# Optimization experiments

Measured on AMD Instinct MI355X. Metric: run time of the kernel, lower is better.

## Reference

```python
import jax, jax.numpy as jnp
import numpy as np

SCORE_THRESHOLD = 0.3
MAX_DET = 300


def _nms_keep(boxes, valid, iou_thresh):
    # Greedy NMS. boxes [N,4] already sorted desc by score and class-offset;
    # valid [N] bool marks entries passing the score threshold.
    x1, y1, x2, y2 = boxes[:, 0], boxes[:, 1], boxes[:, 2], boxes[:, 3]
    areas = jnp.maximum(x2 - x1, 0.0) * jnp.maximum(y2 - y1, 0.0)
    N = boxes.shape[0]
    idx = jnp.arange(N)

    def body(i, keep):
        bi = boxes[i]
        xx1 = jnp.maximum(bi[0], x1)
        yy1 = jnp.maximum(bi[1], y1)
        xx2 = jnp.minimum(bi[2], x2)
        yy2 = jnp.minimum(bi[3], y2)
        inter = jnp.maximum(xx2 - xx1, 0.0) * jnp.maximum(yy2 - yy1, 0.0)
        iou = inter / (areas[i] + areas - inter + 1e-9)
        suppress = (iou > iou_thresh) & (idx > i) & keep[i]
        return keep & (~suppress)

    return jax.lax.fori_loop(0, N, body, valid)


def setup_inputs() -> dict:
    key = jax.random.key(0)
    k1, k2, k3, k4 = jax.random.split(key, 4)
    B, N = 16, 4096
    img = 512.0
    # plausible boxes: centers in [0, 512], sizes in [10, 100]
    cxy = jax.random.uniform(k1, (B, N, 2)) * img
    wh = jax.random.uniform(k2, (B, N, 2)) * 90.0 + 10.0
    boxes = jnp.concatenate([cxy - wh / 2.0, cxy + wh / 2.0], axis=-1)
    scores = jax.random.uniform(k3, (B, N))
    labels = jax.random.randint(k4, (B, N), 0, 2, dtype=jnp.int32)
    nms_thresh = jnp.float32(-0.6)
    class_weights = jnp.ones((2,), jnp.float32)
    return {"boxes": boxes, "scores": scores, "labels": labels,
            "nms_thresh": nms_thresh, "class_weights": class_weights,
            "img_size": 512}


def reference(boxes, scores, labels, nms_thresh, class_weights, img_size):
    B, N, _ = boxes.shape
    fimg = jnp.asarray(img_size, boxes.dtype)
    boxes = jnp.clip(boxes, 0.0, fimg)  # clamp all 4 coords to [0, img_size]
    valid = scores > SCORE_THRESHOLD
    weighted = scores * class_weights[labels]
    # sort each batch by weighted score, invalid entries pushed to the end
    sort_key = jnp.where(valid, weighted, -jnp.inf)
    order = jnp.argsort(-sort_key, axis=1)
    sb = jnp.take_along_axis(boxes, order[..., None], axis=1)   # [B,N,4]
    ss = jnp.take_along_axis(scores, order, axis=1)             # original scores
    sl = jnp.take_along_axis(labels, order, axis=1)
    sv = jnp.take_along_axis(valid, order, axis=1)
    iou_thresh = jax.nn.sigmoid(nms_thresh)
    # batched_nms trick: offset boxes per class so cross-class IoU is 0
    ob = sb + sl.astype(sb.dtype)[..., None] * (fimg + 1.0)
    keep = jax.vmap(_nms_keep, in_axes=(0, 0, None))(ob, sv, iou_thresh)  # [B,N]
    # compact kept detections (score order preserved) into padded [B, MAX_DET]
    rank = jnp.cumsum(keep, axis=1) - 1
    pos = jnp.where(keep & (rank < MAX_DET), rank, MAX_DET)  # overflow slot MAX_DET
    brow = jnp.arange(B)[:, None]
    out_boxes = jnp.zeros((B, MAX_DET + 1, 4), sb.dtype).at[brow, pos].set(sb)[:, :MAX_DET]
    out_scores = jnp.zeros((B, MAX_DET + 1), ss.dtype).at[brow, pos].set(ss)[:, :MAX_DET]
    out_labels = jnp.zeros((B, MAX_DET + 1), sl.dtype).at[brow, pos].set(sl)[:, :MAX_DET]
    out_valid = jnp.zeros((B, MAX_DET + 1), bool).at[brow, pos].set(keep)[:, :MAX_DET]
    return out_boxes, out_scores, out_labels, out_valid
```

## Files before the change

### kernel.cpp

```cpp
#include <hip/hip_runtime.h>
#include <math.h>

#define NBOX   4096
#define NTHR   1024
#define MAXDET 300
#define CAP    3968
#define NWORDS (NBOX / 32)

typedef unsigned long long ull;

__device__ __forceinline__ float clipf(float v, float hi) {
  return fminf(fmaxf(v, 0.0f), hi);
}

__device__ __forceinline__ float getimg(const int* img_i) {
  int iv = *img_i;
  return (iv > 0 && iv < (1 << 24)) ? (float)iv : __int_as_float(iv);
}

#define CSWAP_REG(va, vb, eo, K) { int e_ = wbase + (eo) + lane;                     \
    if ((((e_) & (K)) == 0) ? ((va) < (vb)) : ((va) > (vb))) { ull t_=(va); (va)=(vb); (vb)=t_; } }
#define CSWAP_SHFL(vr, eo, K) { int e_ = wbase + (eo) + lane;                        \
    ull c_ = __shfl_xor((vr), j);                                                    \
    bool km_ = ((((e_) & (K)) == 0) == ((lane & j) == 0));                           \
    (vr) = km_ ? ((vr) > c_ ? (vr) : c_) : ((vr) < c_ ? (vr) : c_); }
#define LOCALPHASES(jmax, K) { for (int j = (jmax); j >= 1; j >>= 1) {               \
    if (j == 128)      { CSWAP_REG(v0, v2, 0, K);  CSWAP_REG(v1, v3, 64, K);  }      \
    else if (j == 64)  { CSWAP_REG(v0, v1, 0, K);  CSWAP_REG(v2, v3, 128, K); }      \
    else { CSWAP_SHFL(v0, 0, K); CSWAP_SHFL(v1, 64, K); CSWAP_SHFL(v2, 128, K); CSWAP_SHFL(v3, 192, K); } } }

__device__ __forceinline__ void emit_one(ull key, int l, int b, int N,
    const float* boxes, const int* labels, float fimg, float offs,
    int* ws_sorted, float4* obox, float* area)
{
  unsigned orig = 0xFFFFFFFFu - (unsigned)(key & 0xFFFFFFFFull);
  ws_sorted[(size_t)b * N + l] = (int)orig;
  const float4* bx4 = (const float4*)(boxes + (size_t)b * N * 4);
  float4 bb = bx4[orig];
  float off = (float)labels[(size_t)b * N + orig] * offs;
  bb.x = clipf(bb.x, fimg) + off;
  bb.y = clipf(bb.y, fimg) + off;
  bb.z = clipf(bb.z, fimg) + off;
  bb.w = clipf(bb.w, fimg) + off;
  obox[(size_t)b * NBOX + l] = bb;
  area[(size_t)b * NBOX + l] = fmaxf(bb.z - bb.x, 0.0f) * fmaxf(bb.w - bb.y, 0.0f);
}

__global__ __launch_bounds__(256)
void sort_seg(const float* __restrict__ scores,
              const int*   __restrict__ labels,
              const float* __restrict__ cls_w,
              ull* __restrict__ ws_keys,
              int* __restrict__ ws_Vseg,
              int N)
{
  __shared__ ull ks[1024];
  __shared__ int cnt;
  const int b = blockIdx.y, s = blockIdx.x;
  const int tid = threadIdx.x, lane = tid & 63, wave = tid >> 6;
  const int wbase = wave * 256;
  const int base  = s * 1024;
  const float* sc = scores + (size_t)b * N;
  const int*   lb = labels + (size_t)b * N;
  if (tid == 0) cnt = 0;

  ull v0, v1, v2, v3;
  int vc = 0;
  #define BUILD(vm, mo) { int l_ = wbase + (mo) + lane; int gi = base + l_;          \
      float sv = sc[gi]; ull key = (ull)(0xFFFFFFFFu - (unsigned)gi);                \
      if (sv > 0.3f) { float w_ = sv * cls_w[lb[gi]]; unsigned ub = __float_as_uint(w_); \
        ub = (ub & 0x80000000u) ? ~ub : (ub | 0x80000000u);                          \
        key |= ((ull)ub << 32); ++vc; }                                              \
      vm = key; }
  BUILD(v0, 0) BUILD(v1, 64) BUILD(v2, 128) BUILD(v3, 192)
  #undef BUILD
  atomicAdd(&cnt, vc);

  for (int k2 = 2; k2 <= 256; k2 <<= 1) { LOCALPHASES(k2 >> 1, k2); }

  #define STV { ks[wbase + lane] = v0; ks[wbase + 64 + lane] = v1;                   \
                ks[wbase + 128 + lane] = v2; ks[wbase + 192 + lane] = v3; }
  #define LDV { v0 = ks[wbase + lane]; v1 = ks[wbase + 64 + lane];                   \
                v2 = ks[wbase + 128 + lane]; v3 = ks[wbase + 192 + lane]; }
  #define CROSS(J, K) { for (int i = tid; i < 1024; i += 256) { int l2 = i ^ (J);    \
      if (l2 > i) { ull a = ks[i], c = ks[l2];                                       \
        if ((((i) & (K)) == 0) ? (a < c) : (a > c)) { ks[i] = c; ks[l2] = a; } } } }

  STV; __syncthreads();
  CROSS(256, 512); __syncthreads();
  LDV; LOCALPHASES(128, 512);
  STV; __syncthreads();
  CROSS(512, 1024); __syncthreads();
  CROSS(256, 1024); __syncthreads();
  LDV; LOCALPHASES(128, 1024);

  ull* kb = ws_keys + (size_t)b * NBOX + base;
  kb[wbase + lane]       = v0;
  kb[wbase + 64 + lane]  = v1;
  kb[wbase + 128 + lane] = v2;
  kb[wbase + 192 + lane] = v3;
  __syncthreads();
  if (tid == 0) ws_Vseg[b * 4 + s] = cnt;
  #undef STV
  #undef LDV
  #undef CROSS
}

__global__ __launch_bounds__(512)
void merge_top(const ull* __restrict__ ws_keys,
               const int* __restrict__ ws_Vseg,
               const float* __restrict__ boxes,
               const int*   __restrict__ labels,
               const int*   __restrict__ img_i,
               int*    __restrict__ ws_sorted,
               int*    __restrict__ ws_V,
               int*    __restrict__ ws_done,
               float4* __restrict__ obox,
               float*  __restrict__ area,
               int N)
{
  __shared__ ull ksh[2][1024];
  const int b = blockIdx.x;
  const int tid = threadIdx.x, lane = tid & 63, wave = tid >> 6;
  const int g = wave >> 2, wv = wave & 3;
  const int wbase = wv * 256;
  const ull* kb = ws_keys + (size_t)b * NBOX;

  ull v0, v1, v2, v3;
  #define PMAX(vm, mo) { int l_ = wbase + (mo) + lane;                               \
      ull a = kb[g * 2048 + l_]; ull c = kb[g * 2048 + 1024 + (1023 - l_)];          \
      vm = (a > c) ? a : c; }
  PMAX(v0, 0) PMAX(v1, 64) PMAX(v2, 128) PMAX(v3, 192)
  #undef PMAX

  #define STVG(arr) { (arr)[wbase + lane] = v0; (arr)[wbase + 64 + lane] = v1;       \
                      (arr)[wbase + 128 + lane] = v2; (arr)[wbase + 192 + lane] = v3; }
  #define LDVG(arr) { v0 = (arr)[wbase + lane]; v1 = (arr)[wbase + 64 + lane];       \
                      v2 = (arr)[wbase + 128 + lane]; v3 = (arr)[wbase + 192 + lane]; }
  #define MCROSS(arr, J) { for (int i = (tid & 255); i < 1024; i += 256) {           \
      int l2 = i ^ (J); if (l2 > i) { ull a = (arr)[i], c = (arr)[l2];               \
        if (a < c) { (arr)[i] = c; (arr)[l2] = a; } } } }

  STVG(ksh[g]); __syncthreads();
  MCROSS(ksh[g], 512); __syncthreads();
  MCROSS(ksh[g], 256); __syncthreads();
  LDVG(ksh[g]); LOCALPHASES(128, 2048);
  STVG(ksh[g]); __syncthreads();

  if (g == 0) {
    #define PMAX2(vm, mo) { int l_ = wbase + (mo) + lane;                            \
        ull a = ksh[0][l_]; ull c = ksh[1][1023 - l_]; vm = (a > c) ? a : c; }
    PMAX2(v0, 0) PMAX2(v1, 64) PMAX2(v2, 128) PMAX2(v3, 192)
    #undef PMAX2
  }
  __syncthreads();
  if (g == 0) STVG(ksh[0]);
  __syncthreads();
  if (tid < 256) MCROSS(ksh[0], 512);
  __syncthreads();
  if (tid < 256) MCROSS(ksh[0], 256);
  __syncthreads();

  if (g == 0) {
    LDVG(ksh[0]); LOCALPHASES(128, 2048);
    float fimg = getimg(img_i);
    float offs = fimg + 1.0f;
    emit_one(v0, wbase + lane,       b, N, boxes, labels, fimg, offs, ws_sorted, obox, area);
    emit_one(v1, wbase + 64 + lane,  b, N, boxes, labels, fimg, offs, ws_sorted, obox, area);
    emit_one(v2, wbase + 128 + lane, b, N, boxes, labels, fimg, offs, ws_sorted, obox, area);
    emit_one(v3, wbase + 192 + lane, b, N, boxes, labels, fimg, offs, ws_sorted, obox, area);
  }
  if (tid == 0) {
    ws_V[b] = ws_Vseg[b * 4] + ws_Vseg[b * 4 + 1] + ws_Vseg[b * 4 + 2] + ws_Vseg[b * 4 + 3];
    ws_done[b] = 0;
  }
  #undef STVG
  #undef LDVG
  #undef MCROSS
}

__global__ __launch_bounds__(256)
void suptr0(const float4* __restrict__ obox,
            const float*  __restrict__ area,
            const float*  __restrict__ nms_th,
            const int*    __restrict__ ws_V,
            ull* __restrict__ trans)
{
  __shared__ float4 rbox[64];
  __shared__ float  rarea[64];
  __shared__ ull    part[4][64];
  const int b = blockIdx.y;
  int rem = blockIdx.x, d = 0;
  while (rem >= d + 1) { rem -= d + 1; ++d; }
  const int jt = d, w = rem;
  const int V = ws_V[b];
  if (jt * 64 >= V) return;
  const int JW = (V + 63) >> 6;
  if (w >= JW) return;

  const int tid = threadIdx.x, wave = tid >> 6, lane = tid & 63;
  double xt = (double)(*nms_th);
  float  th = (float)(1.0 / (1.0 + exp(-xt)));
  const float4* ob = obox + (size_t)b * NBOX;
  const float*  ar = area + (size_t)b * NBOX;

  if (tid < 64) { rbox[tid] = ob[w * 64 + tid]; rarea[tid] = ar[w * 64 + tid]; }
  __syncthreads();

  const int j = jt * 64 + lane;
  const float4 bj = ob[j];
  const float  aj = ar[j];
  ull p = 0;
  #pragma unroll 4
  for (int rr = 0; rr < 16; ++rr) {
    const int r = wave * 16 + rr;
    const int i = w * 64 + r;
    const float4 bi = rbox[r];
    const float  ai = rarea[r];
    float xx1 = fmaxf(bi.x, bj.x);
    float yy1 = fmaxf(bi.y, bj.y);
    float xx2 = fminf(bi.z, bj.z);
    float yy2 = fminf(bi.w, bj.w);
    float inter = fmaxf(xx2 - xx1, 0.0f) * fmaxf(yy2 - yy1, 0.0f);
    float denom = ai + aj;
    denom = denom - inter;
    denom = denom + 1e-9f;
    float iou = inter / denom;
    bool cond = (iou > th) && (j > i);
    p |= cond ? (1ull << r) : 0ull;
  }
  part[wave][lane] = p;
  __syncthreads();
  if (tid < 64)
    trans[(size_t)b * 16 * NBOX + (size_t)w * NBOX + jt * 64 + tid] =
        (part[0][tid] | part[1][tid]) | (part[2][tid] | part[3][tid]);
}

__global__ __launch_bounds__(NTHR)
void resolve0(const float* __restrict__ boxes,
              const float* __restrict__ scores,
              const int*   __restrict__ labels,
              const int*   __restrict__ img_i,
              const int*   __restrict__ ws_V,
              const ull*   __restrict__ trans,
              int* __restrict__ ws_done,
              int* __restrict__ ws_total,
              ull* __restrict__ ws_keptw,
              int* __restrict__ ws_K,
              const int* __restrict__ ws_sorted,
              float* __restrict__ out,
              int B, int N)
{
  __shared__ ull aw[16];
  __shared__ ull kw[16];
  __shared__ int kept_sh[MAXDET];
  __shared__ int flag, fin, Ktot;

  const int b = blockIdx.x;
  const int tid = threadIdx.x, wave = tid >> 6, lane = tid & 63;
  const int V = ws_V[b], JW = (V + 63) >> 6;
  const int j = tid;
  const ull* tb = trans + (size_t)b * 16 * NBOX;

  ull supT[16];
  #pragma unroll
  for (int w = 0; w < 16; ++w)
    supT[w] = (w <= wave) ? tb[(size_t)w * NBOX + j] : 0ull;

  const bool a0 = (j < V);
  { ull bw0 = __ballot(a0); if (lane == 0) aw[wave] = bw0; }
  __syncthreads();

  for (;;) {
    ull s = 0;
    #pragma unroll
    for (int w = 0; w < 16; ++w) s |= aw[w] & supT[w];
    const bool keep = a0 && (s == 0ull);
    const ull bw = __ballot(keep);
    const bool diff = (lane == 0) && (bw != aw[wave]);
    __syncthreads();
    if (tid == 0) flag = 0;
    __syncthreads();
    if (diff) { aw[wave] = bw; flag = 1; }
    __syncthreads();
    if (!flag) break;
  }

  if (wave == 0) {
    ull w64 = (lane < 16) ? aw[lane] : 0ull;
    int pc = __popcll(w64), incl = pc;
    #pragma unroll
    for (int s2 = 1; s2 < 64; s2 <<= 1) { int v = __shfl_up(incl, s2); if (lane >= s2) incl += v; }
    const int totalALL = __shfl(incl, 63);
    const bool fi = (totalALL >= MAXDET) || (16 >= JW);
    if (fi) {
      int cumprev = incl - pc;
      int room = MAXDET - cumprev; if (room < 0) room = 0;
      int nk = (room < pc) ? room : pc;
      if (nk == 0) w64 = 0;
      else while (pc > nk) { int msb = 63 - __builtin_clzll(w64); w64 &= ~(1ull << msb); --pc; }
    }
    if (lane < 16) { kw[lane] = w64; ws_keptw[(size_t)b * 64 + lane] = w64; }
    if (lane == 0) { fin = fi ? 1 : 0; Ktot = (totalALL < MAXDET) ? totalALL : MAXDET; }
  }
  __syncthreads();

  if (!fin) { if (tid == 0) ws_total[b] = Ktot; return; }

  if (wave == 0) {
    ull km = (lane < 16) ? kw[lane] : 0ull;
    int pc = __popcll(km), incl = pc;
    #pragma unroll
    for (int s2 = 1; s2 < 64; s2 <<= 1) { int v = __shfl_up(incl, s2); if (lane >= s2) incl += v; }
    int base = incl - pc;
    while (km) { int l = __builtin_ctzll(km); km &= km - 1; kept_sh[base++] = lane * 64 + l; }
  }
  __syncthreads();

  const int K = Ktot;
  float fimg = getimg(img_i);
  const float* bx = boxes  + (size_t)b * N * 4;
  const float* sc = scores + (size_t)b * N;
  const int*   lb = labels + (size_t)b * N;
  const int*   so = ws_sorted + (size_t)b * N;
  float4* obx = (float4*)out;
  float*  osc = out + (size_t)B * MAXDET * 4;
  float*  olb = osc + (size_t)B * MAXDET;
  float*  ovl = olb + (size_t)B * MAXDET;
  for (int rI = tid; rI < MAXDET; rI += NTHR) {
    size_t slot = (size_t)b * MAXDET + rI;
    if (rI < K) {
      int i    = kept_sh[rI];
      int orig = so[i];
      float4 bb = ((const float4*)bx)[orig];
      bb.x = clipf(bb.x, fimg);
      bb.y = clipf(bb.y, fimg);
      bb.z = clipf(bb.z, fimg);
      bb.w = clipf(bb.w, fimg);
      obx[slot] = bb;
      osc[slot] = sc[orig];
      olb[slot] = (float)lb[orig];
      ovl[slot] = 1.0f;
    } else {
      obx[slot] = make_float4(0.f, 0.f, 0.f, 0.f);
      osc[slot] = 0.0f;
      olb[slot] = 0.0f;
      ovl[slot] = 0.0f;
    }
  }
  if (tid == 0) { ws_K[b] = K; ws_done[b] = 1; }
}

__global__ __launch_bounds__(NTHR)
void cleanup_kernel(const ull* __restrict__ ws_keys,
                    const float* __restrict__ boxes,
                    const float* __restrict__ scores,
                    const int*   __restrict__ labels,
                    const int*   __restrict__ img_i,
                    const float* __restrict__ nms_th,
                    const int* __restrict__ ws_V,
                    int* __restrict__ ws_done,
                    const int* __restrict__ ws_total,
                    const ull* __restrict__ ws_keptw,
                    const float4* __restrict__ obox,
                    int* __restrict__ ws_K,
                    float* __restrict__ out,
                    int B, int N)
{
  __shared__ ull    K[4096];
  __shared__ float4 rb[1024];
  __shared__ float  ra[1024];
  __shared__ float4 kbox[MAXDET];
  __shared__ float  karea[MAXDET];
  __shared__ ull    aw[16];
  __shared__ ull    kw[64];
  __shared__ int    kept_sh[MAXDET];
  __shared__ int    flag, fin, Ktot;

  const int b = blockIdx.x;
  if (ws_done[b]) return;
  const int tid = threadIdx.x, wave = tid >> 6, lane = tid & 63;
  const int V = ws_V[b], JW = (V + 63) >> 6;
  float fimg = getimg(img_i);
  float offs = fimg + 1.0f;
  double xt = (double)(*nms_th);
  float th = (float)(1.0 / (1.0 + exp(-xt)));

  const ull* kb = ws_keys + (size_t)b * NBOX;
  for (int i = tid; i < 4096; i += NTHR) K[i] = kb[i];
  __syncthreads();
  { int i = tid;
    { ull a = K[i], c = K[2047 - i];        if (a < c) { K[i] = c; K[2047 - i] = a; } }
    { ull a = K[2048 + i], c = K[4095 - i]; if (a < c) { K[2048 + i] = c; K[4095 - i] = a; } } }
  __syncthreads();
  for (int j2 = 512; j2 >= 1; j2 >>= 1) {
    for (int idx = tid; idx < 4096; idx += NTHR) {
      int l = idx ^ j2;
      if (l > idx) { ull a = K[idx], c = K[l]; if (a < c) { K[idx] = c; K[l] = a; } } }
    __syncthreads(); }
  for (int m = 0; m < 2; ++m) {
    int i2 = tid + m * NTHR;
    ull a = K[i2], c = K[4095 - i2];
    if (a < c) { K[i2] = c; K[4095 - i2] = a; } }
  __syncthreads();
  for (int j2 = 1024; j2 >= 1; j2 >>= 1) {
    for (int idx = tid; idx < 4096; idx += NTHR) {
      int l = idx ^ j2;
      if (l > idx) { ull a = K[idx], c = K[l]; if (a < c) { K[idx] = c; K[l] = a; } } }
    __syncthreads(); }

  int total = ws_total[b];
  const ull* kwg = ws_keptw + (size_t)b * 64;
  if (tid < 64) kw[tid] = (tid < 16) ? kwg[tid] : 0ull;
  __syncthreads();
  if (wave == 0) {
    ull km = (lane < 16) ? kw[lane] : 0ull;
    int pc = __popcll(km), incl = pc;
    #pragma unroll
    for (int s2 = 1; s2 < 64; s2 <<= 1) { int v = __shfl_up(incl, s2); if (lane >= s2) incl += v; }
    int base = incl - pc;
    while (km) { int l = __builtin_ctzll(km); km &= km - 1; kept_sh[base++] = lane * 64 + l; }
  }
  __syncthreads();
  for (int k = tid; k < total; k += NTHR) {
    float4 bb = obox[(size_t)b * NBOX + kept_sh[k]];
    kbox[k]  = bb;
    karea[k] = fmaxf(bb.z - bb.x, 0.0f) * fmaxf(bb.w - bb.y, 0.0f);
  }
  __syncthreads();

  for (int c = 1; c < 4; ++c) {
    const int t0 = 16 * c, t1 = t0 + 16;
    {
      int gi = t0 * 64 + tid;
      unsigned orig = 0xFFFFFFFFu - (unsigned)(K[gi] & 0xFFFFFFFFull);
      float4 bb = ((const float4*)(boxes + (size_t)b * N * 4))[orig];
      float off = (float)labels[(size_t)b * N + orig] * offs;
      bb.x = clipf(bb.x, fimg) + off;
      bb.y = clipf(bb.y, fimg) + off;
      bb.z = clipf(bb.z, fimg) + off;
      bb.w = clipf(bb.w, fimg) + off;
      rb[tid] = bb;
      ra[tid] = fmaxf(bb.z - bb.x, 0.0f) * fmaxf(bb.w - bb.y, 0.0f);
    }
    __syncthreads();

    const int j = t0 * 64 + tid;
    const float4 bj = rb[tid];
    const float  aj = ra[tid];

    ull supT[16];
    for (int w = 0; w < 16; ++w) {
      ull word = 0;
      if (w <= wave) {
        for (int rr = 0; rr < 64; ++rr) {
          const int lr = w * 64 + rr;
          const float4 bi = rb[lr];
          const float  ai = ra[lr];
          float xx1 = fmaxf(bi.x, bj.x);
          float yy1 = fmaxf(bi.y, bj.y);
          float xx2 = fminf(bi.z, bj.z);
          float yy2 = fminf(bi.w, bj.w);
          float inter = fmaxf(xx2 - xx1, 0.0f) * fmaxf(yy2 - yy1, 0.0f);
          float denom = ai + aj;
          denom = denom - inter;
          denom = denom + 1e-9f;
          float iou = inter / denom;
          bool cond = (iou > th) && (tid > lr);
          word |= cond ? (1ull << rr) : 0ull;
        }
      }
      supT[w] = word;
    }
    bool cat = false;
    for (int k = 0; k < total && !cat; ++k) {
      const float4 bi = kbox[k];
      const float  ai = karea[k];
      float xx1 = fmaxf(bi.x, bj.x);
      float yy1 = fmaxf(bi.y, bj.y);
      float xx2 = fminf(bi.z, bj.z);
      float yy2 = fminf(bi.w, bj.w);
      float inter = fmaxf(xx2 - xx1, 0.0f) * fmaxf(yy2 - yy1, 0.0f);
      float denom = ai + aj;
      denom = denom - inter;
      denom = denom + 1e-9f;
      float iou = inter / denom;
      if (iou > th) cat = true;
    }
    const bool a0 = (j < V) && !cat;
    { ull bw0 = __ballot(a0); if (lane == 0) aw[wave] = bw0; }
    __syncthreads();

    for (;;) {
      ull s = 0;
      #pragma unroll
      for (int w = 0; w < 16; ++w) s |= aw[w] & supT[w];
      const bool keep = a0 && (s == 0ull);
      const ull bw = __ballot(keep);
      const bool diff = (lane == 0) && (bw != aw[wave]);
      __syncthreads();
      if (tid == 0) flag = 0;
      __syncthreads();
      if (diff) { aw[wave] = bw; flag = 1; }
      __syncthreads();
      if (!flag) break;
    }

    if (wave == 0) {
      ull w64 = (lane < 16) ? aw[lane] : 0ull;
      int pc = __popcll(w64), incl = pc;
      #pragma unroll
      for (int s2 = 1; s2 < 64; s2 <<= 1) { int v = __shfl_up(incl, s2); if (lane >= s2) incl += v; }
      const int totalALL = total + __shfl(incl, 63);
      const bool fi = (totalALL >= MAXDET) || (t1 >= JW);
      if (fi) {
        int cumprev = total + incl - pc;
        int room = MAXDET - cumprev; if (room < 0) room = 0;
        int nk = (room < pc) ? room : pc;
        if (nk == 0) { w64 = 0; pc = 0; }
        else while (pc > nk) { int msb = 63 - __builtin_clzll(w64); w64 &= ~(1ull << msb); --pc; }
      }
      if (lane < 16) kw[t0 + lane] = w64;
      if (lane == 0) { fin = fi ? 1 : 0; Ktot = (totalALL < MAXDET) ? totalALL : MAXDET; }
    }
    __syncthreads();

    if (wave == 0) {
      ull km = (lane < 16) ? kw[t0 + lane] : 0ull;
      int pc = __popcll(km), incl = pc;
      #pragma unroll
      for (int s2 = 1; s2 < 64; s2 <<= 1) { int v = __shfl_up(incl, s2); if (lane >= s2) incl += v; }
      int base = total + incl - pc;
      while (km) { int l = __builtin_ctzll(km); km &= km - 1; kept_sh[base++] = (t0 + lane) * 64 + l; }
    }
    __syncthreads();
    const int newtotal = Ktot;
    for (int k = total + tid; k < newtotal; k += NTHR) {
      int lr = kept_sh[k] - t0 * 64;
      kbox[k]  = rb[lr];
      karea[k] = ra[lr];
    }
    total = newtotal;
    __syncthreads();
    if (fin) break;
  }

  const int Kf = total;
  const float* bx = boxes  + (size_t)b * N * 4;
  const float* sc = scores + (size_t)b * N;
  const int*   lb = labels + (size_t)b * N;
  float4* obx = (float4*)out;
  float*  osc = out + (size_t)B * MAXDET * 4;
  float*  olb = osc + (size_t)B * MAXDET;
  float*  ovl = olb + (size_t)B * MAXDET;
  for (int rI = tid; rI < MAXDET; rI += NTHR) {
    size_t slot = (size_t)b * MAXDET + rI;
    if (rI < Kf) {
      int i = kept_sh[rI];
      unsigned orig = 0xFFFFFFFFu - (unsigned)(K[i] & 0xFFFFFFFFull);
      float4 bb = ((const float4*)bx)[orig];
      bb.x = clipf(bb.x, fimg);
      bb.y = clipf(bb.y, fimg);
      bb.z = clipf(bb.z, fimg);
      bb.w = clipf(bb.w, fimg);
      obx[slot] = bb;
      osc[slot] = sc[orig];
      olb[slot] = (float)lb[orig];
      ovl[slot] = 1.0f;
    } else {
      obx[slot] = make_float4(0.f, 0.f, 0.f, 0.f);
      osc[slot] = 0.0f;
      olb[slot] = 0.0f;
      ovl[slot] = 0.0f;
    }
  }
  if (tid == 0) { ws_K[b] = Kf; ws_done[b] = 1; }
}

__global__ __launch_bounds__(NTHR)
void merge_full(const ull* __restrict__ ws_keys,
                const float* __restrict__ boxes,
                const int*   __restrict__ labels,
                const int*   __restrict__ img_i,
                int*    __restrict__ ws_sorted,
                float4* __restrict__ obox,
                float*  __restrict__ area,
                int N)
{
  __shared__ ull K[4096];
  const int b = blockIdx.x;
  const int tid = threadIdx.x;
  const ull* kb = ws_keys + (size_t)b * NBOX;
  for (int i = tid; i < 4096; i += NTHR) K[i] = kb[i];
  __syncthreads();
  { int i = tid;
    { ull a = K[i], c = K[2047 - i];        if (a < c) { K[i] = c; K[2047 - i] = a; } }
    { ull a = K[2048 + i], c = K[4095 - i]; if (a < c) { K[2048 + i] = c; K[4095 - i] = a; } } }
  __syncthreads();
  for (int j = 512; j >= 1; j >>= 1) {
    for (int idx = tid; idx < 4096; idx += NTHR) {
      int l = idx ^ j;
      if (l > idx) { ull a = K[idx], c = K[l]; if (a < c) { K[idx] = c; K[l] = a; } } }
    __syncthreads(); }
  for (int m = 0; m < 2; ++m) {
    int i2 = tid + m * 1024;
    ull a = K[i2], c = K[4095 - i2];
    if (a < c) { K[i2] = c; K[4095 - i2] = a; } }
  __syncthreads();
  for (int j = 1024; j >= 1; j >>= 1) {
    for (int idx = tid; idx < 4096; idx += NTHR) {
      int l = idx ^ j;
      if (l > idx) { ull a = K[idx], c = K[l]; if (a < c) { K[idx] = c; K[l] = a; } } }
    __syncthreads(); }

  float fimg = getimg(img_i);
  float offs = fimg + 1.0f;
  for (int idx = 1024 + tid; idx < 4096; idx += NTHR)
    emit_one(K[idx], idx, b, N, boxes, labels, fimg, offs, ws_sorted, obox, area);
}

struct SMB {
  float4       obox[CAP];
  unsigned int keepw[NWORDS];
  int          kept_pos[MAXDET];
  int          scal[4];
};

__global__ __launch_bounds__(NTHR)
void nms_kernel(const float* __restrict__ boxes,
                const float* __restrict__ scores,
                const int*   __restrict__ labels,
                const float* __restrict__ nms_th,
                const float* __restrict__ cls_w,
                const int*   __restrict__ img_i,
                float* __restrict__ out,
                int B, int N,
                const int* __restrict__ ws_sorted,
                const int* __restrict__ ws_V,
                float4* __restrict__ ws_ovf)
{
  __shared__ SMB sm;
  const int b    = blockIdx.x;
  const int tid  = threadIdx.x;

  const float* bx = boxes  + (size_t)b * N * 4;
  const float* sc = scores + (size_t)b * N;
  const int*   lb = labels + (size_t)b * N;
  const int*   so = ws_sorted + (size_t)b * N;

  float fimg = getimg(img_i);
  float off_scale = fimg + 1.0f;
  double xt = (double)(*nms_th);
  float  th = (float)(1.0 / (1.0 + exp(-xt)));

  const int V = ws_V[b];
  if (tid < 4) sm.scal[tid] = 0;

  for (int m = 0; m < 4; ++m) {
    int i = tid + m * NTHR;
    int orig = so[i];
    float4 bb = ((const float4*)bx)[orig];
    float off = (float)lb[orig] * off_scale;
    bb.x = clipf(bb.x, fimg) + off;
    bb.y = clipf(bb.y, fimg) + off;
    bb.z = clipf(bb.z, fimg) + off;
    bb.w = clipf(bb.w, fimg) + off;
    if (i < CAP) sm.obox[i] = bb;
    else         ws_ovf[(size_t)b * (NBOX - CAP) + (i - CAP)] = bb;
  }
  for (int w = tid; w < NWORDS; w += NTHR) {
    int lo = w * 32;
    unsigned val;
    if      (V >= lo + 32) val = 0xFFFFFFFFu;
    else if (V <= lo)      val = 0u;
    else                   val = (1u << (V - lo)) - 1u;
    sm.keepw[w] = val;
  }
  __syncthreads();

  const int nt = (V + 63) >> 6;
  int TR = 0;
  for (int t = 0; t < nt; ++t) {
    if (tid < 64) {
      int i0 = t * 64;
      int me = i0 + tid;
      float4 bb = (me < CAP) ? sm.obox[me]
                             : ws_ovf[(size_t)b * (NBOX - CAP) + (me - CAP)];
      float arJ = fmaxf(bb.z - bb.x, 0.0f) * fmaxf(bb.w - bb.y, 0.0f);
      ull supby = 0;
      for (int l = 0; l < 64; ++l) {
        int i = i0 + l;
        float4 bi = (i < CAP) ? sm.obox[i]
                              : ws_ovf[(size_t)b * (NBOX - CAP) + (i - CAP)];
        float ai = fmaxf(bi.z - bi.x, 0.0f) * fmaxf(bi.w - bi.y, 0.0f);
        float xx1 = fmaxf(bi.x, bb.x);
        float yy1 = fmaxf(bi.y, bb.y);
        float xx2 = fminf(bi.z, bb.z);
        float yy2 = fminf(bi.w, bb.w);
        float inter = fmaxf(xx2 - xx1, 0.0f) * fmaxf(yy2 - yy1, 0.0f);
        float denom = ai + arJ;
        denom = denom - inter;
        denom = denom + 1e-9f;
        float iou = inter / denom;
        if (iou > th) supby |= (1ull << l);
      }
      ull alive = ((ull)sm.keepw[2 * t + 1] << 32) | sm.keepw[2 * t];
      ull rem = alive;
      while (rem) {
        int l = __builtin_ctzll(rem);
        rem &= rem - 1;
        ull sup = __ballot((supby >> l) & 1ull);
        sup &= ((~1ull) << l);
        sup &= alive;
        alive &= ~sup;
        rem   &= ~sup;
      }
      if (tid == 0) {
        sm.keepw[2 * t]     = (unsigned)alive;
        sm.keepw[2 * t + 1] = (unsigned)(alive >> 32);
        atomicAdd(&sm.scal[1], __builtin_popcountll(alive));
      }
    }
    __syncthreads();
    TR = t + 1;
    if (sm.scal[1] >= MAXDET) break;

    int jstart = (t + 1) * 64;
    if (jstart < V) {
      ull alive = ((ull)sm.keepw[2 * t + 1] << 32) | sm.keepw[2 * t];
      if (alive) {
        for (int j = jstart + tid; j < V; j += NTHR) {
          unsigned wj = sm.keepw[j >> 5];
          if (!((wj >> (j & 31)) & 1u)) continue;
          float4 bj = (j < CAP) ? sm.obox[j]
                                : ws_ovf[(size_t)b * (NBOX - CAP) + (j - CAP)];
          float aj = fmaxf(bj.z - bj.x, 0.0f) * fmaxf(bj.w - bj.y, 0.0f);
          ull rem = alive;
          bool suppressed = false;
          while (rem) {
            int l = __builtin_ctzll(rem);
            rem &= rem - 1;
            int i = t * 64 + l;
            float4 bi = (i < CAP) ? sm.obox[i]
                                  : ws_ovf[(size_t)b * (NBOX - CAP) + (i - CAP)];
            float ai = fmaxf(bi.z - bi.x, 0.0f) * fmaxf(bi.w - bi.y, 0.0f);
            float xx1 = fmaxf(bi.x, bj.x);
            float yy1 = fmaxf(bi.y, bj.y);
            float xx2 = fminf(bi.z, bj.z);
            float yy2 = fminf(bi.w, bj.w);
            float inter = fmaxf(xx2 - xx1, 0.0f) * fmaxf(yy2 - yy1, 0.0f);
            float denom = ai + aj;
            denom = denom - inter;
            denom = denom + 1e-9f;
            float iou = inter / denom;
            if (iou > th) { suppressed = true; break; }
          }
          if (suppressed) atomicAnd(&sm.keepw[j >> 5], ~(1u << (j & 31)));
        }
      }
    }
    __syncthreads();
  }

  if (tid < NWORDS && tid >= TR * 2) sm.keepw[tid] = 0;
  __syncthreads();
  if (tid == 0) {
    int r = 0;
    for (int w = 0; w < NWORDS && r < MAXDET; ++w) {
      unsigned bits = sm.keepw[w];
      while (bits && r < MAXDET) {
        int l = __builtin_ctz(bits);
        bits &= bits - 1;
        sm.kept_pos[r++] = w * 32 + l;
      }
    }
    sm.scal[3] = r;
  }
  __syncthreads();
  const int K = sm.scal[3];

  float4* obx = (float4*)out;
  float*  osc = out + (size_t)B * MAXDET * 4;
  float*  olb = osc + (size_t)B * MAXDET;
  float*  ovl = olb + (size_t)B * MAXDET;
  for (int r = tid; r < MAXDET; r += NTHR) {
    size_t slot = (size_t)b * MAXDET + r;
    if (r < K) {
      int i    = sm.kept_pos[r];
      int orig = so[i];
      float4 bb = ((const float4*)bx)[orig];
      bb.x = clipf(bb.x, fimg);
      bb.y = clipf(bb.y, fimg);
      bb.z = clipf(bb.z, fimg);
      bb.w = clipf(bb.w, fimg);
      obx[slot] = bb;
      osc[slot] = sc[orig];
      olb[slot] = (float)lb[orig];
      ovl[slot] = 1.0f;
    } else {
      obx[slot] = make_float4(0.f, 0.f, 0.f, 0.f);
      osc[slot] = 0.0f;
      olb[slot] = 0.0f;
      ovl[slot] = 0.0f;
    }
  }
}

extern "C" void kernel_launch(void* const* d_in, const int* in_sizes, int n_in,
                              void* d_out, int out_size, void* d_ws, size_t ws_size,
                              hipStream_t stream) {
  const float* boxes      = (const float*)d_in[0];
  const float* scores     = (const float*)d_in[1];
  const int*   labels     = (const int*)d_in[2];
  const float* nms_thresh = (const float*)d_in[3];
  const float* cls_w      = (const float*)d_in[4];
  const int*   img_sz     = (const int*)d_in[5];

  int B = out_size / (MAXDET * 7);
  int N = in_sizes[1] / B;

  size_t off_sorted = 0;
  size_t off_V      = (off_sorted + (size_t)B * N * 4 + 255) & ~(size_t)255;
  size_t off_Vseg   = off_V + (size_t)B * 4;
  size_t off_done   = off_Vseg + (size_t)B * 16;
  size_t off_total  = off_done + (size_t)B * 4;
  size_t off_Kf     = off_total + (size_t)B * 4;
  size_t off_kw     = (off_Kf + (size_t)B * 4 + 255) & ~(size_t)255;
  size_t off_obox   = (off_kw + (size_t)B * 64 * 8 + 255) & ~(size_t)255;
  size_t off_area   = off_obox + (size_t)B * NBOX * 16;
  size_t off_keys   = (off_area + (size_t)B * NBOX * 4 + 255) & ~(size_t)255;
  size_t off_tr     = (off_keys + (size_t)B * NBOX * 8 + 255) & ~(size_t)255;
  size_t sz_tr      = (size_t)B * 16 * NBOX * 8;
  size_t need_fast  = off_tr + sz_tr;

  int*    ws_sorted = (int*)((char*)d_ws + off_sorted);
  int*    ws_V      = (int*)((char*)d_ws + off_V);
  int*    ws_Vseg   = (int*)((char*)d_ws + off_Vseg);
  int*    ws_done   = (int*)((char*)d_ws + off_done);
  int*    ws_total  = (int*)((char*)d_ws + off_total);
  int*    ws_K      = (int*)((char*)d_ws + off_Kf);
  ull*    ws_keptw  = (ull*)((char*)d_ws + off_kw);
  float4* obox      = (float4*)((char*)d_ws + off_obox);
  float*  area      = (float*)((char*)d_ws + off_area);
  ull*    ws_keys   = (ull*)((char*)d_ws + off_keys);
  ull*    trans     = (ull*)((char*)d_ws + off_tr);

  if (ws_size >= need_fast && N == NBOX) {
    sort_seg<<<dim3(4, B), dim3(256), 0, stream>>>(scores, labels, cls_w,
                                                   ws_keys, ws_Vseg, N);
    merge_top<<<dim3(B), dim3(512), 0, stream>>>(ws_keys, ws_Vseg, boxes, labels,
                                                 img_sz, ws_sorted, ws_V, ws_done,
                                                 obox, area, N);
    suptr0<<<dim3(136, B), dim3(256), 0, stream>>>(
        obox, area, nms_thresh, ws_V, trans);
    resolve0<<<dim3(B), dim3(NTHR), 0, stream>>>(
        boxes, scores, labels, img_sz, ws_V, trans,
        ws_done, ws_total, ws_keptw, ws_K, ws_sorted, (float*)d_out, B, N);
    cleanup_kernel<<<dim3(B), dim3(NTHR), 0, stream>>>(
        ws_keys, boxes, scores, labels, img_sz, nms_thresh, ws_V,
        ws_done, ws_total, ws_keptw, obox, ws_K, (float*)d_out, B, N);
  } else {
    sort_seg<<<dim3(4, B), dim3(256), 0, stream>>>(scores, labels, cls_w,
                                                   ws_keys, ws_Vseg, N);
    merge_top<<<dim3(B), dim3(512), 0, stream>>>(ws_keys, ws_Vseg, boxes, labels,
                                                 img_sz, ws_sorted, ws_V, ws_done,
                                                 obox, area, N);
    merge_full<<<dim3(B), dim3(NTHR), 0, stream>>>(
        ws_keys, boxes, labels, img_sz, ws_sorted, obox, area, N);
    float4* ws_ovf = (float4*)((char*)d_ws + off_keys);
    nms_kernel<<<dim3(B), dim3(NTHR), 0, stream>>>(boxes, scores, labels,
                                                   nms_thresh, cls_w, img_sz,
                                                   (float*)d_out, B, N,
                                                   ws_sorted, ws_V, ws_ovf);
  }
}
```

Baseline: 58.56 us.

## Fuse segment sort and top merge into one kernel; double-buffer resolve flags

Merges the per-segment bitonic sort and the top-k merge into a single 1024-thread block per batch, so the merge reads sorted keys from shared memory instead of global memory and one kernel launch is removed. Valid counts now stay in shared memory rather than going through a workspace array. Separately, the resolve loop uses double-buffered alive masks and __syncthreads_or, which cuts three barriers per iteration down to one. The trade-off is only 16 blocks for the sort stage (previously 64), which lowers parallelism, and a larger shared memory footprint.

```diff
diff --git a/kernel.cpp b/kernel.cpp
--- a/kernel.cpp
+++ b/kernel.cpp
@@ -46,27 +46,40 @@
   area[(size_t)b * NBOX + l] = fmaxf(bb.z - bb.x, 0.0f) * fmaxf(bb.w - bb.y, 0.0f);
 }
 
-__global__ __launch_bounds__(256)
-void sort_seg(const float* __restrict__ scores,
-              const int*   __restrict__ labels,
-              const float* __restrict__ cls_w,
-              ull* __restrict__ ws_keys,
-              int* __restrict__ ws_Vseg,
-              int N)
+__global__ __launch_bounds__(NTHR)
+void sort_merge(const float* __restrict__ scores,
+                const int*   __restrict__ labels,
+                const float* __restrict__ cls_w,
+                const float* __restrict__ boxes,
+                const int*   __restrict__ img_i,
+                ull* __restrict__ ws_keys,
+                int* __restrict__ ws_sorted,
+                int* __restrict__ ws_V,
+                int* __restrict__ ws_done,
+                float4* __restrict__ obox,
+                float*  __restrict__ area,
+                int N)
 {
-  __shared__ ull ks[1024];
-  __shared__ int cnt;
-  const int b = blockIdx.y, s = blockIdx.x;
-  const int tid = threadIdx.x, lane = tid & 63, wave = tid >> 6;
-  const int wbase = wave * 256;
-  const int base  = s * 1024;
+  __shared__ ull ks[4096];
+  __shared__ ull ksh[2][1024];
+  __shared__ int cnt[4];
+
+  const int b = blockIdx.x;
+  const int tid = threadIdx.x;
+  const int lane = tid & 63;
+  const int wave = tid >> 6;
+  const int wv = wave & 3;
+  const int wbase = wv * 256;
+  const int s = tid >> 8;
+  const int gtid = tid & 255;
   const float* sc = scores + (size_t)b * N;
   const int*   lb = labels + (size_t)b * N;
-  if (tid == 0) cnt = 0;
+
+  if (tid < 4) cnt[tid] = 0;
 
   ull v0, v1, v2, v3;
   int vc = 0;
-  #define BUILD(vm, mo) { int l_ = wbase + (mo) + lane; int gi = base + l_;          \
+  #define BUILD(vm, mo) { int l_ = wbase + (mo) + lane; int gi = s * 1024 + l_;      \
       float sv = sc[gi]; ull key = (ull)(0xFFFFFFFFu - (unsigned)gi);                \
       if (sv > 0.3f) { float w_ = sv * cls_w[lb[gi]]; unsigned ub = __float_as_uint(w_); \
         ub = (ub & 0x80000000u) ? ~ub : (ub | 0x80000000u);                          \
@@ -74,64 +87,40 @@
       vm = key; }
   BUILD(v0, 0) BUILD(v1, 64) BUILD(v2, 128) BUILD(v3, 192)
   #undef BUILD
-  atomicAdd(&cnt, vc);
 
   for (int k2 = 2; k2 <= 256; k2 <<= 1) { LOCALPHASES(k2 >> 1, k2); }
 
-  #define STV { ks[wbase + lane] = v0; ks[wbase + 64 + lane] = v1;                   \
-                ks[wbase + 128 + lane] = v2; ks[wbase + 192 + lane] = v3; }
-  #define LDV { v0 = ks[wbase + lane]; v1 = ks[wbase + 64 + lane];                   \
-                v2 = ks[wbase + 128 + lane]; v3 = ks[wbase + 192 + lane]; }
-  #define CROSS(J, K) { for (int i = tid; i < 1024; i += 256) { int l2 = i ^ (J);    \
-      if (l2 > i) { ull a = ks[i], c = ks[l2];                                       \
-        if ((((i) & (K)) == 0) ? (a < c) : (a > c)) { ks[i] = c; ks[l2] = a; } } } }
+  #define STV { ks[s*1024 + wbase + lane] = v0; ks[s*1024 + wbase + 64 + lane] = v1; \
+                ks[s*1024 + wbase + 128 + lane] = v2; ks[s*1024 + wbase + 192 + lane] = v3; }
+  #define LDV { v0 = ks[s*1024 + wbase + lane]; v1 = ks[s*1024 + wbase + 64 + lane]; \
+                v2 = ks[s*1024 + wbase + 128 + lane]; v3 = ks[s*1024 + wbase + 192 + lane]; }
+  #define CROSS(J, K) { for (int i = gtid; i < 1024; i += 256) { int l2 = i ^ (J);   \
+      if (l2 > i) { ull a = ks[s*1024 + i], c = ks[s*1024 + l2];                     \
+        if ((((i) & (K)) == 0) ? (a < c) : (a > c)) { ks[s*1024 + i] = c; ks[s*1024 + l2] = a; } } } }
 
   STV; __syncthreads();
+  atomicAdd(&cnt[s], vc);
   CROSS(256, 512); __syncthreads();
   LDV; LOCALPHASES(128, 512);
   STV; __syncthreads();
   CROSS(512, 1024); __syncthreads();
   CROSS(256, 1024); __syncthreads();
   LDV; LOCALPHASES(128, 1024);
-
-  ull* kb = ws_keys + (size_t)b * NBOX + base;
-  kb[wbase + lane]       = v0;
-  kb[wbase + 64 + lane]  = v1;
-  kb[wbase + 128 + lane] = v2;
-  kb[wbase + 192 + lane] = v3;
-  __syncthreads();
-  if (tid == 0) ws_Vseg[b * 4 + s] = cnt;
+  STV;
+  {
+    ull* kb = ws_keys + (size_t)b * NBOX + s * 1024;
+    kb[wbase + lane]       = v0;
+    kb[wbase + 64 + lane]  = v1;
+    kb[wbase + 128 + lane] = v2;
+    kb[wbase + 192 + lane] = v3;
+  }
+  __syncthreads();
   #undef STV
   #undef LDV
   #undef CROSS
-}
-
-__global__ __launch_bounds__(512)
-void merge_top(const ull* __restrict__ ws_keys,
-               const int* __restrict__ ws_Vseg,
-               const float* __restrict__ boxes,
-               const int*   __restrict__ labels,
-               const int*   __restrict__ img_i,
-               int*    __restrict__ ws_sorted,
-               int*    __restrict__ ws_V,
-               int*    __restrict__ ws_done,
-               float4* __restrict__ obox,
-               float*  __restrict__ area,
-               int N)
-{
-  __shared__ ull ksh[2][1024];
-  const int b = blockIdx.x;
-  const int tid = threadIdx.x, lane = tid & 63, wave = tid >> 6;
-  const int g = wave >> 2, wv = wave & 3;
-  const int wbase = wv * 256;
-  const ull* kb = ws_keys + (size_t)b * NBOX;
-
-  ull v0, v1, v2, v3;
-  #define PMAX(vm, mo) { int l_ = wbase + (mo) + lane;                               \
-      ull a = kb[g * 2048 + l_]; ull c = kb[g * 2048 + 1024 + (1023 - l_)];          \
-      vm = (a > c) ? a : c; }
-  PMAX(v0, 0) PMAX(v1, 64) PMAX(v2, 128) PMAX(v3, 192)
-  #undef PMAX
+
+  const bool act = (tid < 512);
+  const int g2 = wave >> 2;
 
   #define STVG(arr) { (arr)[wbase + lane] = v0; (arr)[wbase + 64 + lane] = v1;       \
                       (arr)[wbase + 128 + lane] = v2; (arr)[wbase + 192 + lane] = v3; }
@@ -141,27 +130,37 @@
       int l2 = i ^ (J); if (l2 > i) { ull a = (arr)[i], c = (arr)[l2];               \
         if (a < c) { (arr)[i] = c; (arr)[l2] = a; } } } }
 
-  STVG(ksh[g]); __syncthreads();
-  MCROSS(ksh[g], 512); __syncthreads();
-  MCROSS(ksh[g], 256); __syncthreads();
-  LDVG(ksh[g]); LOCALPHASES(128, 2048);
-  STVG(ksh[g]); __syncthreads();
-
-  if (g == 0) {
+  if (act) {
+    #define PMAX(vm, mo) { int l_ = wbase + (mo) + lane;                             \
+        ull a = ks[g2 * 2048 + l_]; ull c = ks[g2 * 2048 + 1024 + (1023 - l_)];      \
+        vm = (a > c) ? a : c; }
+    PMAX(v0, 0) PMAX(v1, 64) PMAX(v2, 128) PMAX(v3, 192)
+    #undef PMAX
+    STVG(ksh[g2]);
+  }
+  __syncthreads();
+  if (act) MCROSS(ksh[g2], 512);
+  __syncthreads();
+  if (act) MCROSS(ksh[g2], 256);
+  __syncthreads();
+  if (act) { LDVG(ksh[g2]); LOCALPHASES(128, 2048); STVG(ksh[g2]); }
+  __syncthreads();
+
+  if (g2 == 0) {
     #define PMAX2(vm, mo) { int l_ = wbase + (mo) + lane;                            \
         ull a = ksh[0][l_]; ull c = ksh[1][1023 - l_]; vm = (a > c) ? a : c; }
     PMAX2(v0, 0) PMAX2(v1, 64) PMAX2(v2, 128) PMAX2(v3, 192)
     #undef PMAX2
   }
   __syncthreads();
-  if (g == 0) STVG(ksh[0]);
+  if (g2 == 0) STVG(ksh[0]);
   __syncthreads();
   if (tid < 256) MCROSS(ksh[0], 512);
   __syncthreads();
   if (tid < 256) MCROSS(ksh[0], 256);
   __syncthreads();
 
-  if (g == 0) {
+  if (g2 == 0) {
     LDVG(ksh[0]); LOCALPHASES(128, 2048);
     float fimg = getimg(img_i);
     float offs = fimg + 1.0f;
@@ -171,7 +170,7 @@
     emit_one(v3, wbase + 192 + lane, b, N, boxes, labels, fimg, offs, ws_sorted, obox, area);
   }
   if (tid == 0) {
-    ws_V[b] = ws_Vseg[b * 4] + ws_Vseg[b * 4 + 1] + ws_Vseg[b * 4 + 2] + ws_Vseg[b * 4 + 3];
+    ws_V[b] = cnt[0] + cnt[1] + cnt[2] + cnt[3];
     ws_done[b] = 0;
   }
   #undef STVG
@@ -251,10 +250,10 @@
               float* __restrict__ out,
               int B, int N)
 {
-  __shared__ ull aw[16];
+  __shared__ ull awb[2][16];
   __shared__ ull kw[16];
   __shared__ int kept_sh[MAXDET];
-  __shared__ int flag, fin, Ktot;
+  __shared__ int fin, Ktot;
 
   const int b = blockIdx.x;
   const int tid = threadIdx.x, wave = tid >> 6, lane = tid & 63;
@@ -268,26 +267,25 @@
     supT[w] = (w <= wave) ? tb[(size_t)w * NBOX + j] : 0ull;
 
   const bool a0 = (j < V);
-  { ull bw0 = __ballot(a0); if (lane == 0) aw[wave] = bw0; }
-  __syncthreads();
-
+  { ull bw0 = __ballot(a0); if (lane == 0) awb[0][wave] = bw0; }
+  __syncthreads();
+
+  int cur = 0;
   for (;;) {
     ull s = 0;
     #pragma unroll
-    for (int w = 0; w < 16; ++w) s |= aw[w] & supT[w];
+    for (int w = 0; w < 16; ++w) s |= awb[cur][w] & supT[w];
     const bool keep = a0 && (s == 0ull);
     const ull bw = __ballot(keep);
-    const bool diff = (lane == 0) && (bw != aw[wave]);
-    __syncthreads();
-    if (tid == 0) flag = 0;
-    __syncthreads();
-    if (diff) { aw[wave] = bw; flag = 1; }
-    __syncthreads();
-    if (!flag) break;
+    const bool mych = (lane == 0) && (bw != awb[cur][wave]);
+    if (lane == 0) awb[cur ^ 1][wave] = bw;
+    const int changed = __syncthreads_or((int)mych);
+    if (!changed) break;
+    cur ^= 1;
   }
 
   if (wave == 0) {
-    ull w64 = (lane < 16) ? aw[lane] : 0ull;
+    ull w64 = (lane < 16) ? awb[cur][lane] : 0ull;
     int pc = __popcll(w64), incl = pc;
     #pragma unroll
     for (int s2 = 1; s2 < 64; s2 <<= 1) { int v = __shfl_up(incl, s2); if (lane >= s2) incl += v; }
@@ -821,8 +819,7 @@
 
   size_t off_sorted = 0;
   size_t off_V      = (off_sorted + (size_t)B * N * 4 + 255) & ~(size_t)255;
-  size_t off_Vseg   = off_V + (size_t)B * 4;
-  size_t off_done   = off_Vseg + (size_t)B * 16;
+  size_t off_done   = off_V + (size_t)B * 4;
   size_t off_total  = off_done + (size_t)B * 4;
   size_t off_Kf     = off_total + (size_t)B * 4;
   size_t off_kw     = (off_Kf + (size_t)B * 4 + 255) & ~(size_t)255;
@@ -835,7 +832,6 @@
 
   int*    ws_sorted = (int*)((char*)d_ws + off_sorted);
   int*    ws_V      = (int*)((char*)d_ws + off_V);
-  int*    ws_Vseg   = (int*)((char*)d_ws + off_Vseg);
   int*    ws_done   = (int*)((char*)d_ws + off_done);
   int*    ws_total  = (int*)((char*)d_ws + off_total);
   int*    ws_K      = (int*)((char*)d_ws + off_Kf);
@@ -846,11 +842,9 @@
   ull*    trans     = (ull*)((char*)d_ws + off_tr);
 
   if (ws_size >= need_fast && N == NBOX) {
-    sort_seg<<<dim3(4, B), dim3(256), 0, stream>>>(scores, labels, cls_w,
-                                                   ws_keys, ws_Vseg, N);
-    merge_top<<<dim3(B), dim3(512), 0, stream>>>(ws_keys, ws_Vseg, boxes, labels,
-                                                 img_sz, ws_sorted, ws_V, ws_done,
-                                                 obox, area, N);
+    sort_merge<<<dim3(B), dim3(NTHR), 0, stream>>>(
+        scores, labels, cls_w, boxes, img_sz,
+        ws_keys, ws_sorted, ws_V, ws_done, obox, area, N);
     suptr0<<<dim3(136, B), dim3(256), 0, stream>>>(
         obox, area, nms_thresh, ws_V, trans);
     resolve0<<<dim3(B), dim3(NTHR), 0, stream>>>(
@@ -860,11 +854,9 @@
         ws_keys, boxes, scores, labels, img_sz, nms_thresh, ws_V,
         ws_done, ws_total, ws_keptw, obox, ws_K, (float*)d_out, B, N);
   } else {
-    sort_seg<<<dim3(4, B), dim3(256), 0, stream>>>(scores, labels, cls_w,
-                                                   ws_keys, ws_Vseg, N);
-    merge_top<<<dim3(B), dim3(512), 0, stream>>>(ws_keys, ws_Vseg, boxes, labels,
-                                                 img_sz, ws_sorted, ws_V, ws_done,
-                                                 obox, area, N);
+    sort_merge<<<dim3(B), dim3(NTHR), 0, stream>>>(
+        scores, labels, cls_w, boxes, img_sz,
+        ws_keys, ws_sorted, ws_V, ws_done, obox, area, N);
     merge_full<<<dim3(B), dim3(NTHR), 0, stream>>>(
         ws_keys, boxes, labels, img_sz, ws_sorted, obox, area, N);
     float4* ws_ovf = (float4*)((char*)d_ws + off_keys);
```

New measurement: 62.53 us. 1.07x slower.
